# Optimization experiments

Hardware: AMD Instinct MI355X
Metric: run time of the kernel (lower is better)

## Reference

```python
import jax, jax.numpy as jnp
import numpy as np

D_MODEL = 1024
TEMPERATURE = 1.0

def setup_inputs() -> dict:
    key = jax.random.key(0)
    ks = jax.random.split(key, 9)
    B, NQ, NK, D = 4, 2048, 2048, D_MODEL
    s = 1.0 / np.sqrt(D)
    return {
        "Q": jax.random.normal(ks[0], (B, NQ, D), jnp.float32),
        "K": jax.random.normal(ks[1], (B, NK, D), jnp.float32),
        "V": jax.random.normal(ks[2], (B, NK, D), jnp.float32),
        "Wq": jax.random.normal(ks[3], (D, D), jnp.float32) * s,
        "bq": jax.random.normal(ks[4], (D,), jnp.float32) * 0.01,
        "Wk": jax.random.normal(ks[5], (D, D), jnp.float32) * s,
        "bk": jax.random.normal(ks[6], (D,), jnp.float32) * 0.01,
        "Wv": jax.random.normal(ks[7], (D, D), jnp.float32) * s,
        "bv": jax.random.normal(ks[8], (D,), jnp.float32) * 0.01,
    }

def reference(Q, K, V, Wq, bq, Wk, bk, Wv, bv):
    # torch nn.Linear: y = x @ W.T + b
    Qp = Q @ Wq.T + bq  # [B, NQ, D]
    Kp = K @ Wk.T + bk  # [B, NK, D]
    Vp = V @ Wv.T + bv  # [B, NK, D]

    # use_kl=True branch, vectorized:
    # kl[b,i,j] = D_KL(softmax(Kp[b,j]) || softmax(Qp[b,i]))
    #           = sum_d pK*(log pK - log pQ) = -H(pK_j) - pK_j . log pQ_i
    logpQ = jax.nn.log_softmax(Qp, axis=-1)  # [B, NQ, D]
    logpK = jax.nn.log_softmax(Kp, axis=-1)  # [B, NK, D]
    pK = jnp.exp(logpK)
    neg_ent_K = jnp.sum(pK * logpK, axis=-1)            # [B, NK], = -H(pK)
    cross = jnp.einsum('bjd,bid->bij', pK, logpQ)       # [B, NQ, NK]
    kl = neg_ent_K[:, None, :] - cross                  # [B, NQ, NK]
    scores = -kl / TEMPERATURE

    attn = jax.nn.softmax(scores, axis=-1)              # [B, NQ, NK]
    out = jnp.einsum('bij,bjd->bid', attn, Vp)          # [B, NQ, D]
    return out, attn
```

## Files before the change

### kernel.cpp

```cpp
#include <hip/hip_runtime.h>
#include <math.h>

#define D_MODEL 1024
#define NQS 2048
#define NKS 2048
#define BATCH 4

typedef __attribute__((ext_vector_type(8))) short bf16x8;
typedef __attribute__((ext_vector_type(4))) float f32x4;

#define AS1 __attribute__((address_space(1)))
#define AS3 __attribute__((address_space(3)))

__device__ __forceinline__ unsigned short f2bf(float f) {
  unsigned u = __builtin_bit_cast(unsigned, f);
  u = (u + 0x7FFF + ((u >> 16) & 1)) >> 16;
  return (unsigned short)u;
}
__device__ __forceinline__ float bf2f(unsigned short s) {
  return __builtin_bit_cast(float, ((unsigned)s) << 16);
}

__global__ __launch_bounds__(256) void cvt3_k(
    const float* __restrict__ s0, const float* __restrict__ s1,
    const float* __restrict__ s2, short* __restrict__ d0,
    short* __restrict__ d1, short* __restrict__ d2, int n8)
{
  const int z = blockIdx.z;
  const float* src = z == 0 ? s0 : (z == 1 ? s1 : s2);
  short* dst = z == 0 ? d0 : (z == 1 ? d1 : d2);
  int i = blockIdx.x * 256 + threadIdx.x;
  if (i >= n8) return;
  const float4 a = *(const float4*)&src[(long)i * 8];
  const float4 b = *(const float4*)&src[(long)i * 8 + 4];
  bf16x8 o;
  o[0] = (short)f2bf(a.x); o[1] = (short)f2bf(a.y);
  o[2] = (short)f2bf(a.z); o[3] = (short)f2bf(a.w);
  o[4] = (short)f2bf(b.x); o[5] = (short)f2bf(b.y);
  o[6] = (short)f2bf(b.z); o[7] = (short)f2bf(b.w);
  *(bf16x8*)&dst[(long)i * 8] = o;
}

__device__ __forceinline__ void gemm_tile_body(
    const short* __restrict__ Ab, const short* __restrict__ Bb,
    const float* __restrict__ bias, float bscale, float* __restrict__ Cf,
    short* __restrict__ Cbf, int N, int K, int gm, int gn)
{
  __shared__ short As[2][128 * 32];
  __shared__ short Bs[2][128 * 32];
  const int t = threadIdx.x;
  const int lane = t & 63, w = t >> 6;
  const int wm = w >> 1, wn = w & 1;

  const int srow = lane >> 2, sq = lane & 3;
  const short* gA0 = Ab + (long)(gm + w * 32 + srow) * K + sq * 8;
  const short* gA1 = Ab + (long)(gm + w * 32 + 16 + srow) * K + sq * 8;
  const short* gB0 = Bb + (long)(gn + w * 32 + srow) * K + sq * 8;
  const short* gB1 = Bb + (long)(gn + w * 32 + 16 + srow) * K + sq * 8;
  const int seg0 = (w * 2 + 0) * 512, seg1 = (w * 2 + 1) * 512;

  const int frow = lane & 15, fq = lane >> 4;

  f32x4 acc[4][4] = {};

  for (int k0 = 0; k0 < K; k0 += 64) {
#pragma unroll
    for (int p = 0; p < 2; ++p) {
      const int ko = k0 + p * 32;
      __builtin_amdgcn_global_load_lds((const AS1 void*)(gA0 + ko),
                                       (AS3 void*)(&As[p][seg0]), 16, 0, 0);
      __builtin_amdgcn_global_load_lds((const AS1 void*)(gA1 + ko),
                                       (AS3 void*)(&As[p][seg1]), 16, 0, 0);
      __builtin_amdgcn_global_load_lds((const AS1 void*)(gB0 + ko),
                                       (AS3 void*)(&Bs[p][seg0]), 16, 0, 0);
      __builtin_amdgcn_global_load_lds((const AS1 void*)(gB1 + ko),
                                       (AS3 void*)(&Bs[p][seg1]), 16, 0, 0);
    }
    __syncthreads();
#pragma unroll
    for (int p = 0; p < 2; ++p) {
      bf16x8 af[4], bfm[4];
#pragma unroll
      for (int mi = 0; mi < 4; ++mi)
        af[mi] =
            *(const bf16x8*)&As[p][(wm * 64 + mi * 16 + frow) * 32 + fq * 8];
#pragma unroll
      for (int ni = 0; ni < 4; ++ni)
        bfm[ni] =
            *(const bf16x8*)&Bs[p][(wn * 64 + ni * 16 + frow) * 32 + fq * 8];
#pragma unroll
      for (int mi = 0; mi < 4; ++mi)
#pragma unroll
        for (int ni = 0; ni < 4; ++ni)
          acc[mi][ni] = __builtin_amdgcn_mfma_f32_16x16x32_bf16(
              af[mi], bfm[ni], acc[mi][ni], 0, 0, 0);
    }
    __syncthreads();
  }

  float bb[4];
#pragma unroll
  for (int ni = 0; ni < 4; ++ni)
    bb[ni] = bias ? bias[gn + wn * 64 + ni * 16 + frow] * bscale : 0.f;

#pragma unroll
  for (int mi = 0; mi < 4; ++mi) {
#pragma unroll
    for (int r = 0; r < 4; ++r) {
      const long row = gm + wm * 64 + mi * 16 + fq * 4 + r;
#pragma unroll
      for (int ni = 0; ni < 4; ++ni) {
        const long col = gn + wn * 64 + ni * 16 + frow;
        float v = acc[mi][ni][r] + bb[ni];
        if (Cf) Cf[row * (long)N + col] = v;
        else    Cbf[row * (long)N + col] = (short)f2bf(v);
      }
    }
  }
}

__global__ __launch_bounds__(256, 4) void mfma_abt_k(
    const short* __restrict__ A, const short* __restrict__ B,
    const float* __restrict__ bias, float bscale, float* __restrict__ Cf,
    short* __restrict__ Cbf, int N, int K, long sA, long sB, long sC,
    long sBias, int swap)
{
  const int bz = blockIdx.z;
  const int gm = (swap ? blockIdx.x : blockIdx.y) * 128;
  const int gn = (swap ? blockIdx.y : blockIdx.x) * 128;
  gemm_tile_body(A + (long)bz * sA, B + (long)bz * sB,
                 bias ? bias + (long)bz * sBias : nullptr, bscale,
                 Cf ? Cf + (long)bz * sC : nullptr,
                 Cbf ? Cbf + (long)bz * sC : nullptr, N, K, gm, gn);
}


#define STAGE_HALF(gbase, hoff, kofs, region)                                \
  do {                                                                       \
    __builtin_amdgcn_global_load_lds(                                        \
        (const AS1 void*)((gbase) + (long)(hoff) * K + (kofs)),              \
        (AS3 void*)((region) + w * 512), 16, 0, 0);                          \
    __builtin_amdgcn_global_load_lds(                                        \
        (const AS1 void*)((gbase) + (long)((hoff) + 64) * K + (kofs)),       \
        (AS3 void*)((region) + 4096 + w * 512), 16, 0, 0);                   \
  } while (0)

#define MFMA_Q(AF, BF, MO, NO)                                        \
  do {                                                                \
    __builtin_amdgcn_s_setprio(1);                                    \
    _Pragma("unroll") for (int kk = 0; kk < 2; ++kk)                  \
        _Pragma("unroll") for (int mi = 0; mi < 4; ++mi)              \
            _Pragma("unroll") for (int ni = 0; ni < 2; ++ni)          \
                acc[(MO) + mi][(NO) + ni] =                           \
                    __builtin_amdgcn_mfma_f32_16x16x32_bf16(          \
                        AF[mi][kk], BF[ni][kk], acc[(MO) + mi][(NO) + ni], \
                        0, 0, 0);                                     \
    __builtin_amdgcn_s_setprio(0);                                    \
  } while (0)

template <int PI>
__device__ __forceinline__ void tile4(short (&As)[2][2][8192],
                                      short (&Bs)[2][2][8192],
                                      const short* gA, const short* gB,
                                      f32x4 (&acc)[8][4],
                                      bf16x8 (&aA)[4][2], bf16x8 (&aB)[4][2],
                                      bf16x8 (&b0r)[2][2], bf16x8 (&b1r)[2][2],
                                      int tau, int NT, int K, int w, int wm,
                                      int wn, int frow, int fq, int fr7)
{
  bf16x8 (&b_cur)[2][2] = PI ? b1r : b0r;
  bf16x8 (&b_alt)[2][2] = PI ? b0r : b1r;
  const short* Ah  = &As[PI][wm][0];
  const short* Bh  = &Bs[PI][wn >> 1][0];
  const short* Ahn = &As[1 - PI][wm][0];
  const short* Bhn = &Bs[1 - PI][wn >> 1][0];
  const int bofs = (wn & 1) * 64;
  const int x0 = (fq ^ fr7) * 8;
  const int x1 = ((4 + fq) ^ fr7) * 8;

#pragma unroll
  for (int mi = 0; mi < 4; ++mi) {
    aB[mi][0] = *(const bf16x8*)&Ah[(64 + mi * 16 + frow) * 64 + x0];
    aB[mi][1] = *(const bf16x8*)&Ah[(64 + mi * 16 + frow) * 64 + x1];
  }
#pragma unroll
  for (int ni = 0; ni < 2; ++ni) {
    b_alt[ni][0] = *(const bf16x8*)&Bh[(bofs + 32 + ni * 16 + frow) * 64 + x0];
    b_alt[ni][1] = *(const bf16x8*)&Bh[(bofs + 32 + ni * 16 + frow) * 64 + x1];
  }
  __builtin_amdgcn_s_barrier();
  MFMA_Q(aA, b_cur, 0, 0);
  __builtin_amdgcn_s_barrier();
  MFMA_Q(aA, b_alt, 0, 2);
  __builtin_amdgcn_s_barrier();
  MFMA_Q(aB, b_alt, 4, 2);
  __builtin_amdgcn_s_barrier();

  asm volatile("s_waitcnt vmcnt(0)" ::: "memory");
  if (tau + 1 < NT) {
#pragma unroll
    for (int mi = 0; mi < 4; ++mi) {
      aA[mi][0] = *(const bf16x8*)&Ahn[(mi * 16 + frow) * 64 + x0];
      aA[mi][1] = *(const bf16x8*)&Ahn[(mi * 16 + frow) * 64 + x1];
    }
#pragma unroll
    for (int ni = 0; ni < 2; ++ni) {
      b_alt[ni][0] = *(const bf16x8*)&Bhn[(bofs + ni * 16 + frow) * 64 + x0];
      b_alt[ni][1] = *(const bf16x8*)&Bhn[(bofs + ni * 16 + frow) * 64 + x1];
    }
  }
  if (tau + 2 < NT) {
    const int kt2 = (tau + 2) << 6;
    STAGE_HALF(gA, 0,   kt2, &As[PI][0][0]);
    STAGE_HALF(gA, 128, kt2, &As[PI][1][0]);
    STAGE_HALF(gB, 0,   kt2, &Bs[PI][0][0]);
    STAGE_HALF(gB, 128, kt2, &Bs[PI][1][0]);
  }
  __builtin_amdgcn_s_barrier();
  MFMA_Q(aB, b_cur, 4, 0);
  __builtin_amdgcn_s_barrier();
}

__device__ __forceinline__ void gemm256_body(
    const short* __restrict__ A, const short* __restrict__ B,
    const float* __restrict__ bias, float bscale, float* __restrict__ Cf,
    short* __restrict__ Cbf, int N, int K, int gm, int gn)
{
  __shared__ short As[2][2][8192];
  __shared__ short Bs[2][2][8192];
  const int t = threadIdx.x;
  const int w = t >> 6, l = t & 63;
  const int wm = w >> 2, wn = w & 3;
  const int frow = l & 15, fq = l >> 4, fr7 = l & 7;
  const int srow0 = w * 8 + (l >> 3);
  const int sslot = (l & 7) ^ (l >> 3);

  const short* gA = A + (long)(gm + srow0) * K + sslot * 8;
  const short* gB = B + (long)(gn + srow0) * K + sslot * 8;

  const int bofs = (wn & 1) * 64;
  const int x0 = (fq ^ fr7) * 8, x1 = ((4 + fq) ^ fr7) * 8;

  f32x4 acc[8][4] = {};
  bf16x8 aA[4][2], aB[4][2], b0r[2][2], b1r[2][2];

  STAGE_HALF(gA, 0,   0,  &As[0][0][0]);
  STAGE_HALF(gA, 128, 0,  &As[0][1][0]);
  STAGE_HALF(gB, 0,   0,  &Bs[0][0][0]);
  STAGE_HALF(gB, 128, 0,  &Bs[0][1][0]);
  STAGE_HALF(gA, 0,   64, &As[1][0][0]);
  STAGE_HALF(gA, 128, 64, &As[1][1][0]);
  STAGE_HALF(gB, 0,   64, &Bs[1][0][0]);
  STAGE_HALF(gB, 128, 64, &Bs[1][1][0]);
  asm volatile("s_waitcnt vmcnt(8)" ::: "memory");
  __builtin_amdgcn_s_barrier();

#pragma unroll
  for (int mi = 0; mi < 4; ++mi) {
    aA[mi][0] = *(const bf16x8*)&As[0][wm][(mi * 16 + frow) * 64 + x0];
    aA[mi][1] = *(const bf16x8*)&As[0][wm][(mi * 16 + frow) * 64 + x1];
  }
#pragma unroll
  for (int ni = 0; ni < 2; ++ni) {
    b0r[ni][0] =
        *(const bf16x8*)&Bs[0][wn >> 1][(bofs + ni * 16 + frow) * 64 + x0];
    b0r[ni][1] =
        *(const bf16x8*)&Bs[0][wn >> 1][(bofs + ni * 16 + frow) * 64 + x1];
  }

  const int NT = K >> 6;
  for (int tau = 0; tau < NT; tau += 2) {
    tile4<0>(As, Bs, gA, gB, acc, aA, aB, b0r, b1r, tau, NT, K, w, wm, wn,
             frow, fq, fr7);
    tile4<1>(As, Bs, gA, gB, acc, aA, aB, b0r, b1r, tau + 1, NT, K, w, wm,
             wn, frow, fq, fr7);
  }

  float bb[4];
#pragma unroll
  for (int Ni = 0; Ni < 4; ++Ni)
    bb[Ni] = bias ? bias[gn + wn * 64 + Ni * 16 + frow] * bscale : 0.f;

#pragma unroll
  for (int Mi = 0; Mi < 8; ++Mi) {
#pragma unroll
    for (int r = 0; r < 4; ++r) {
      const long row = gm + wm * 128 + Mi * 16 + fq * 4 + r;
#pragma unroll
      for (int Ni = 0; Ni < 4; ++Ni) {
        const long col = gn + wn * 64 + Ni * 16 + frow;
        float v = acc[Mi][Ni][r] + bb[Ni];
        if (Cf) Cf[row * (long)N + col] = v;
        else    Cbf[row * (long)N + col] = (short)f2bf(v);
      }
    }
  }
}

__global__ __launch_bounds__(512, 2) void mfma8_abt_k(
    const short* __restrict__ A, const short* __restrict__ B,
    const float* __restrict__ bias, float bscale, float* __restrict__ Cf,
    short* __restrict__ Cbf, int N, int K, long sA, long sB, long sC,
    long sBias, int swap)
{
  const int bz = blockIdx.z;
  const int gm = (swap ? blockIdx.x : blockIdx.y) * 256;
  const int gn = (swap ? blockIdx.y : blockIdx.x) * 256;
  gemm256_body(A + (long)bz * sA, B + (long)bz * sB,
               bias ? bias + (long)bz * sBias : nullptr, bscale,
               Cf ? Cf + (long)bz * sC : nullptr,
               Cbf ? Cbf + (long)bz * sC : nullptr, N, K, gm, gn);
}

__global__ __launch_bounds__(512, 2) void mfma8_proj_k(
    const short* __restrict__ Xq, const short* __restrict__ Xk,
    const short* __restrict__ Xv, const short* __restrict__ Wq,
    const short* __restrict__ Wk, const short* __restrict__ Wv,
    const float* __restrict__ bq, const float* __restrict__ bk,
    const float* __restrict__ bv, short* __restrict__ Oq,
    short* __restrict__ Ok, short* __restrict__ Ov)
{
  const int z = blockIdx.z;
  const short* X = z == 0 ? Xq : (z == 1 ? Xk : Xv);
  const short* W = z == 0 ? Wq : (z == 1 ? Wk : Wv);
  const float* bias = z == 0 ? bq : (z == 1 ? bk : bv);
  short* O = z == 0 ? Oq : (z == 1 ? Ok : Ov);
  gemm256_body(X, W, bias, 1.0f, nullptr, O, D_MODEL, D_MODEL,
               blockIdx.x * 256, blockIdx.y * 256);
}

__global__ __launch_bounds__(256) void kstats_k(short* __restrict__ KP,
                                                float* __restrict__ negent)
{
  __shared__ float red[4];
  const long row = blockIdx.x;
  short* x = KP + row * (long)D_MODEL;
  const int t = threadIdx.x;
  short4 raw = *(const short4*)&x[t * 4];
  float v0 = bf2f((unsigned short)raw.x), v1 = bf2f((unsigned short)raw.y);
  float v2 = bf2f((unsigned short)raw.z), v3 = bf2f((unsigned short)raw.w);
  float m = fmaxf(fmaxf(v0, v1), fmaxf(v2, v3));
  for (int o = 32; o; o >>= 1) m = fmaxf(m, __shfl_xor(m, o));
  if ((t & 63) == 0) red[t >> 6] = m;
  __syncthreads();
  m = fmaxf(fmaxf(red[0], red[1]), fmaxf(red[2], red[3]));
  __syncthreads();
  float e0 = __expf(v0 - m), e1 = __expf(v1 - m), e2 = __expf(v2 - m),
        e3 = __expf(v3 - m);
  float s = e0 + e1 + e2 + e3;
  for (int o = 32; o; o >>= 1) s += __shfl_xor(s, o);
  if ((t & 63) == 0) red[t >> 6] = s;
  __syncthreads();
  s = red[0] + red[1] + red[2] + red[3];
  __syncthreads();
  const float inv = 1.0f / s;
  const float lse = m + __logf(s);
  float p0 = e0 * inv, p1 = e1 * inv, p2 = e2 * inv, p3 = e3 * inv;
  float ne = p0 * (v0 - lse) + p1 * (v1 - lse) + p2 * (v2 - lse) +
             p3 * (v3 - lse);
  for (int o = 32; o; o >>= 1) ne += __shfl_xor(ne, o);
  if ((t & 63) == 0) red[t >> 6] = ne;
  __syncthreads();
  if (t == 0) negent[row] = red[0] + red[1] + red[2] + red[3];
  short4 pw;
  pw.x = (short)f2bf(p0); pw.y = (short)f2bf(p1);
  pw.z = (short)f2bf(p2); pw.w = (short)f2bf(p3);
  *(short4*)&x[t * 4] = pw;
}

__global__ __launch_bounds__(256) void asoftmax_k(float* __restrict__ S,
                                                  short* __restrict__ Sbf)
{
  __shared__ float red[4];
  const long row = blockIdx.x;
  float* x = S + row * (long)NKS;
  short* y = Sbf + row * (long)NKS;
  const int t = threadIdx.x;
  float4 v0 = *(const float4*)&x[t * 4];
  float4 v1 = *(const float4*)&x[1024 + t * 4];
  float m = fmaxf(fmaxf(fmaxf(v0.x, v0.y), fmaxf(v0.z, v0.w)),
                  fmaxf(fmaxf(v1.x, v1.y), fmaxf(v1.z, v1.w)));
  for (int o = 32; o; o >>= 1) m = fmaxf(m, __shfl_xor(m, o));
  if ((t & 63) == 0) red[t >> 6] = m;
  __syncthreads();
  m = fmaxf(fmaxf(red[0], red[1]), fmaxf(red[2], red[3]));
  __syncthreads();
  float4 e0 = {__expf(v0.x - m), __expf(v0.y - m), __expf(v0.z - m),
               __expf(v0.w - m)};
  float4 e1 = {__expf(v1.x - m), __expf(v1.y - m), __expf(v1.z - m),
               __expf(v1.w - m)};
  float s = e0.x + e0.y + e0.z + e0.w + e1.x + e1.y + e1.z + e1.w;
  for (int o = 32; o; o >>= 1) s += __shfl_xor(s, o);
  if ((t & 63) == 0) red[t >> 6] = s;
  __syncthreads();
  s = red[0] + red[1] + red[2] + red[3];
  const float inv = 1.0f / s;
  float4 p0 = {e0.x * inv, e0.y * inv, e0.z * inv, e0.w * inv};
  float4 p1 = {e1.x * inv, e1.y * inv, e1.z * inv, e1.w * inv};
  *(float4*)&x[t * 4] = p0;
  *(float4*)&x[1024 + t * 4] = p1;
  short4 b0, b1;
  b0.x = (short)f2bf(p0.x); b0.y = (short)f2bf(p0.y);
  b0.z = (short)f2bf(p0.z); b0.w = (short)f2bf(p0.w);
  b1.x = (short)f2bf(p1.x); b1.y = (short)f2bf(p1.y);
  b1.z = (short)f2bf(p1.z); b1.w = (short)f2bf(p1.w);
  *(short4*)&y[t * 4] = b0;
  *(short4*)&y[1024 + t * 4] = b1;
}

__global__ __launch_bounds__(256) void transpose_k(const short* __restrict__ src,
                                                   short* __restrict__ dst)
{
  __shared__ short tile[64][68];
  const int j0 = blockIdx.x * 64;
  const int d0 = blockIdx.y * 64;
  const int t = threadIdx.x;
  const int r = t >> 2, c = t & 3;
#pragma unroll
  for (int i = 0; i < 4; ++i)
    *(short4*)&tile[r][c * 16 + i * 4] =
        *(const short4*)&src[(long)(j0 + r) * D_MODEL + d0 + c * 16 + i * 4];
  __syncthreads();
  const long b = j0 >> 11;
  const int jj = j0 & 2047;
#pragma unroll
  for (int i = 0; i < 4; ++i) {
    short4 o;
    o.x = tile[c * 16 + i * 4 + 0][r];
    o.y = tile[c * 16 + i * 4 + 1][r];
    o.z = tile[c * 16 + i * 4 + 2][r];
    o.w = tile[c * 16 + i * 4 + 3][r];
    *(short4*)&dst[b * ((long)D_MODEL * NKS) + (long)(d0 + r) * NKS + jj +
                   c * 16 + i * 4] = o;
  }
}

extern "C" void kernel_launch(void* const* d_in, const int* in_sizes, int n_in,
                              void* d_out, int out_size, void* d_ws,
                              size_t ws_size, hipStream_t stream)
{
  const float* Q = (const float*)d_in[0];
  const float* K = (const float*)d_in[1];
  const float* V = (const float*)d_in[2];
  const float* Wq = (const float*)d_in[3];
  const float* bq = (const float*)d_in[4];
  const float* Wk = (const float*)d_in[5];
  const float* bk = (const float*)d_in[6];
  const float* Wv = (const float*)d_in[7];
  const float* bv = (const float*)d_in[8];

  float* out = (float*)d_out;
  float* attn = out + (long)BATCH * NQS * D_MODEL;

  const long SZ = (long)BATCH * NQS * D_MODEL;
  short* ws = (short*)d_ws;
  short* Qbf = ws;
  short* Kbf = ws + SZ;
  short* Vbf = ws + 2 * SZ;
  short* Qp  = ws + 3 * SZ;
  short* pK  = ws + 4 * SZ;
  short* Vp  = ws + 5 * SZ;
  float* negent = (float*)(ws + 6 * SZ);
  short* attn_bf = ws;
  short* Vpt = ws + 2 * SZ;

  short* Wqb = (short*)attn;
  short* Wkb = Wqb + (long)D_MODEL * D_MODEL;
  short* Wvb = Wkb + (long)D_MODEL * D_MODEL;

  dim3 blk(256), blk8(512);
  const int n8x = (int)(SZ / 8);
  const int n8w = D_MODEL * D_MODEL / 8;

  cvt3_k<<<dim3(n8x / 256, 1, 3), blk, 0, stream>>>(Q, K, V, Qbf, Kbf, Vbf,
                                                    n8x);
  cvt3_k<<<dim3(n8w / 256, 1, 3), blk, 0, stream>>>(Wq, Wk, Wv, Wqb, Wkb, Wvb,
                                                    n8w);

  dim3 gp((BATCH * NQS) / 256, D_MODEL / 256, 3);
  mfma8_proj_k<<<gp, blk8, 0, stream>>>(Qbf, Kbf, Vbf, Wqb, Wkb, Wvb, bq, bk,
                                        bv, Qp, pK, Vp);

  kstats_k<<<dim3(BATCH * NKS), blk, 0, stream>>>(pK, negent);

  transpose_k<<<dim3((BATCH * NKS) / 64, D_MODEL / 64), blk, 0, stream>>>(Vp,
                                                                          Vpt);

  dim3 gs(NKS / 256, NQS / 256, BATCH);
  mfma8_abt_k<<<gs, blk8, 0, stream>>>(
      Qp, pK, negent, -1.0f, attn, nullptr, NKS, D_MODEL,
      (long)NQS * D_MODEL, (long)NKS * D_MODEL, (long)NQS * NKS, NKS, 0);

  asoftmax_k<<<dim3(BATCH * NQS), blk, 0, stream>>>(attn, attn_bf);

  dim3 go(NQS / 128, D_MODEL / 128, BATCH);
  mfma_abt_k<<<go, blk, 0, stream>>>(
      attn_bf, Vpt, nullptr, 0.f, out, nullptr, D_MODEL, NKS,
      (long)NQS * NKS, (long)D_MODEL * NKS, (long)NQS * D_MODEL, 0, 1);
}
```

Measured before the change: 411.1 us.

## Restructure GEMM main loop into 4-phase interleaved staging of A and B tiles

Reworks the 256x256 bf16 GEMM pipeline so that each k-tile is split into four phases. Each phase does LDS fragment reads, issues a quarter of the global-to-LDS prefetches, and runs one MFMA quadrant. A is now prefetched one tile ahead and B two tiles ahead, instead of both two ahead. Register fragments are now local to each tile, which cuts cross-iteration register pressure. The aim is to spread memory traffic evenly between MFMA bursts and reduce the stall at the end-of-tile vmcnt(0), at the cost of a shorter A prefetch distance and different LDS buffer-reuse hazards.

```diff
diff --git a/kernel.cpp b/kernel.cpp
--- a/kernel.cpp
+++ b/kernel.cpp
@@ -145,79 +145,76 @@
         (AS3 void*)((region) + 4096 + w * 512), 16, 0, 0);                   \
   } while (0)
 
-#define MFMA_Q(AF, BF, MO, NO)                                        \
-  do {                                                                \
-    __builtin_amdgcn_s_setprio(1);                                    \
-    _Pragma("unroll") for (int kk = 0; kk < 2; ++kk)                  \
-        _Pragma("unroll") for (int mi = 0; mi < 4; ++mi)              \
-            _Pragma("unroll") for (int ni = 0; ni < 2; ++ni)          \
-                acc[(MO) + mi][(NO) + ni] =                           \
-                    __builtin_amdgcn_mfma_f32_16x16x32_bf16(          \
+#define MFMA_Q(AF, BF, MO, NO)                                             \
+  do {                                                                     \
+    __builtin_amdgcn_s_setprio(1);                                         \
+    _Pragma("unroll") for (int kk = 0; kk < 2; ++kk)                       \
+        _Pragma("unroll") for (int mi = 0; mi < 4; ++mi)                   \
+            _Pragma("unroll") for (int ni = 0; ni < 2; ++ni)               \
+                acc[(MO) + mi][(NO) + ni] =                                \
+                    __builtin_amdgcn_mfma_f32_16x16x32_bf16(               \
                         AF[mi][kk], BF[ni][kk], acc[(MO) + mi][(NO) + ni], \
-                        0, 0, 0);                                     \
-    __builtin_amdgcn_s_setprio(0);                                    \
+                        0, 0, 0);                                          \
+    __builtin_amdgcn_s_setprio(0);                                         \
   } while (0)
 
 template <int PI>
 __device__ __forceinline__ void tile4(short (&As)[2][2][8192],
                                       short (&Bs)[2][2][8192],
                                       const short* gA, const short* gB,
-                                      f32x4 (&acc)[8][4],
-                                      bf16x8 (&aA)[4][2], bf16x8 (&aB)[4][2],
-                                      bf16x8 (&b0r)[2][2], bf16x8 (&b1r)[2][2],
-                                      int tau, int NT, int K, int w, int wm,
-                                      int wn, int frow, int fq, int fr7)
-{
-  bf16x8 (&b_cur)[2][2] = PI ? b1r : b0r;
-  bf16x8 (&b_alt)[2][2] = PI ? b0r : b1r;
-  const short* Ah  = &As[PI][wm][0];
-  const short* Bh  = &Bs[PI][wn >> 1][0];
-  const short* Ahn = &As[1 - PI][wm][0];
-  const short* Bhn = &Bs[1 - PI][wn >> 1][0];
+                                      f32x4 (&acc)[8][4], int tau, int NT,
+                                      int K, int w, int wm, int wn, int frow,
+                                      int fq, int fr7)
+{
+  const int kt1 = (tau + 1) << 6, kt2 = (tau + 2) << 6;
+  const short* Ah = &As[PI][wm][0];
+  const short* Bh = &Bs[PI][wn >> 1][0];
   const int bofs = (wn & 1) * 64;
   const int x0 = (fq ^ fr7) * 8;
   const int x1 = ((4 + fq) ^ fr7) * 8;
 
+  bf16x8 aR[4][2], b0r[2][2], b1r[2][2];
+
 #pragma unroll
   for (int mi = 0; mi < 4; ++mi) {
-    aB[mi][0] = *(const bf16x8*)&Ah[(64 + mi * 16 + frow) * 64 + x0];
-    aB[mi][1] = *(const bf16x8*)&Ah[(64 + mi * 16 + frow) * 64 + x1];
+    aR[mi][0] = *(const bf16x8*)&Ah[(mi * 16 + frow) * 64 + x0];
+    aR[mi][1] = *(const bf16x8*)&Ah[(mi * 16 + frow) * 64 + x1];
   }
 #pragma unroll
   for (int ni = 0; ni < 2; ++ni) {
-    b_alt[ni][0] = *(const bf16x8*)&Bh[(bofs + 32 + ni * 16 + frow) * 64 + x0];
-    b_alt[ni][1] = *(const bf16x8*)&Bh[(bofs + 32 + ni * 16 + frow) * 64 + x1];
-  }
-  __builtin_amdgcn_s_barrier();
-  MFMA_Q(aA, b_cur, 0, 0);
-  __builtin_amdgcn_s_barrier();
-  MFMA_Q(aA, b_alt, 0, 2);
-  __builtin_amdgcn_s_barrier();
-  MFMA_Q(aB, b_alt, 4, 2);
-  __builtin_amdgcn_s_barrier();
-
-  asm volatile("s_waitcnt vmcnt(0)" ::: "memory");
-  if (tau + 1 < NT) {
-#pragma unroll
-    for (int mi = 0; mi < 4; ++mi) {
-      aA[mi][0] = *(const bf16x8*)&Ahn[(mi * 16 + frow) * 64 + x0];
-      aA[mi][1] = *(const bf16x8*)&Ahn[(mi * 16 + frow) * 64 + x1];
-    }
-#pragma unroll
-    for (int ni = 0; ni < 2; ++ni) {
-      b_alt[ni][0] = *(const bf16x8*)&Bhn[(bofs + ni * 16 + frow) * 64 + x0];
-      b_alt[ni][1] = *(const bf16x8*)&Bhn[(bofs + ni * 16 + frow) * 64 + x1];
-    }
-  }
-  if (tau + 2 < NT) {
-    const int kt2 = (tau + 2) << 6;
-    STAGE_HALF(gA, 0,   kt2, &As[PI][0][0]);
-    STAGE_HALF(gA, 128, kt2, &As[PI][1][0]);
-    STAGE_HALF(gB, 0,   kt2, &Bs[PI][0][0]);
-    STAGE_HALF(gB, 128, kt2, &Bs[PI][1][0]);
-  }
-  __builtin_amdgcn_s_barrier();
-  MFMA_Q(aB, b_cur, 4, 0);
+    b0r[ni][0] = *(const bf16x8*)&Bh[(bofs + ni * 16 + frow) * 64 + x0];
+    b0r[ni][1] = *(const bf16x8*)&Bh[(bofs + ni * 16 + frow) * 64 + x1];
+  }
+  if (tau + 1 < NT) STAGE_HALF(gA, 0, kt1, &As[1 - PI][0][0]);
+  __builtin_amdgcn_s_barrier();
+  MFMA_Q(aR, b0r, 0, 0);
+  __builtin_amdgcn_s_barrier();
+
+#pragma unroll
+  for (int ni = 0; ni < 2; ++ni) {
+    b1r[ni][0] = *(const bf16x8*)&Bh[(bofs + 32 + ni * 16 + frow) * 64 + x0];
+    b1r[ni][1] = *(const bf16x8*)&Bh[(bofs + 32 + ni * 16 + frow) * 64 + x1];
+  }
+  if (tau + 1 < NT) STAGE_HALF(gA, 128, kt1, &As[1 - PI][1][0]);
+  __builtin_amdgcn_s_barrier();
+  MFMA_Q(aR, b1r, 0, 2);
+  __builtin_amdgcn_s_barrier();
+
+#pragma unroll
+  for (int mi = 0; mi < 4; ++mi) {
+    aR[mi][0] = *(const bf16x8*)&Ah[(64 + mi * 16 + frow) * 64 + x0];
+    aR[mi][1] = *(const bf16x8*)&Ah[(64 + mi * 16 + frow) * 64 + x1];
+  }
+  if (tau + 2 < NT) STAGE_HALF(gB, 0, kt2, &Bs[PI][0][0]);
+  __builtin_amdgcn_s_barrier();
+  MFMA_Q(aR, b1r, 4, 2);
+  __builtin_amdgcn_s_barrier();
+
+  if (tau + 2 < NT) STAGE_HALF(gB, 128, kt2, &Bs[PI][1][0]);
+  __builtin_amdgcn_s_barrier();
+  MFMA_Q(aR, b0r, 4, 0);
+  if (tau + 2 < NT) asm volatile("s_waitcnt vmcnt(4)" ::: "memory");
+  else              asm volatile("s_waitcnt vmcnt(0)" ::: "memory");
   __builtin_amdgcn_s_barrier();
 }
 
@@ -238,42 +235,21 @@
   const short* gA = A + (long)(gm + srow0) * K + sslot * 8;
   const short* gB = B + (long)(gn + srow0) * K + sslot * 8;
 
-  const int bofs = (wn & 1) * 64;
-  const int x0 = (fq ^ fr7) * 8, x1 = ((4 + fq) ^ fr7) * 8;
-
   f32x4 acc[8][4] = {};
-  bf16x8 aA[4][2], aB[4][2], b0r[2][2], b1r[2][2];
 
   STAGE_HALF(gA, 0,   0,  &As[0][0][0]);
   STAGE_HALF(gA, 128, 0,  &As[0][1][0]);
   STAGE_HALF(gB, 0,   0,  &Bs[0][0][0]);
   STAGE_HALF(gB, 128, 0,  &Bs[0][1][0]);
-  STAGE_HALF(gA, 0,   64, &As[1][0][0]);
-  STAGE_HALF(gA, 128, 64, &As[1][1][0]);
   STAGE_HALF(gB, 0,   64, &Bs[1][0][0]);
   STAGE_HALF(gB, 128, 64, &Bs[1][1][0]);
-  asm volatile("s_waitcnt vmcnt(8)" ::: "memory");
-  __builtin_amdgcn_s_barrier();
-
-#pragma unroll
-  for (int mi = 0; mi < 4; ++mi) {
-    aA[mi][0] = *(const bf16x8*)&As[0][wm][(mi * 16 + frow) * 64 + x0];
-    aA[mi][1] = *(const bf16x8*)&As[0][wm][(mi * 16 + frow) * 64 + x1];
-  }
-#pragma unroll
-  for (int ni = 0; ni < 2; ++ni) {
-    b0r[ni][0] =
-        *(const bf16x8*)&Bs[0][wn >> 1][(bofs + ni * 16 + frow) * 64 + x0];
-    b0r[ni][1] =
-        *(const bf16x8*)&Bs[0][wn >> 1][(bofs + ni * 16 + frow) * 64 + x1];
-  }
+  asm volatile("s_waitcnt vmcnt(4)" ::: "memory");
+  __builtin_amdgcn_s_barrier();
 
   const int NT = K >> 6;
   for (int tau = 0; tau < NT; tau += 2) {
-    tile4<0>(As, Bs, gA, gB, acc, aA, aB, b0r, b1r, tau, NT, K, w, wm, wn,
-             frow, fq, fr7);
-    tile4<1>(As, Bs, gA, gB, acc, aA, aB, b0r, b1r, tau + 1, NT, K, w, wm,
-             wn, frow, fq, fr7);
+    tile4<0>(As, Bs, gA, gB, acc, tau, NT, K, w, wm, wn, frow, fq, fr7);
+    tile4<1>(As, Bs, gA, gB, acc, tau + 1, NT, K, w, wm, wn, frow, fq, fr7);
   }
 
   float bb[4];
```

Result: faster. 382.4 us (-7.0%).
